# Performance work log

Hardware: AMD Instinct MI355X
Metric: run time of the kernel (lower is better)

The kernel has to match this reference:

```python
import jax, jax.numpy as jnp
import numpy as np

N_USER, N_TX, E = 50000, 50000, 600000
D_USER, D_TX, D_ALIGN, HID, OUT = 128, 64, 128, 256, 128


def setup_inputs() -> dict:
    key = jax.random.key(0)
    ks = jax.random.split(key, 16)
    s = 0.05
    return {
        "x_user": jax.random.normal(ks[0], (N_USER, D_USER), jnp.float32),
        "x_tx": jax.random.normal(ks[1], (N_TX, D_TX), jnp.float32),
        "edge_user_tx": jax.random.randint(ks[2], (2, E), 0, N_USER),
        "edge_tx_user": jax.random.randint(ks[3], (2, E), 0, N_TX),
        "W_align_user": jax.random.normal(ks[4], (D_USER, D_ALIGN), jnp.float32) * s,
        "b_align_user": jnp.zeros((D_ALIGN,), jnp.float32),
        "W_align_tx": jax.random.normal(ks[5], (D_TX, D_ALIGN), jnp.float32) * s,
        "b_align_tx": jnp.zeros((D_ALIGN,), jnp.float32),
        "eps_ut": jnp.zeros((), jnp.float32),
        "eps_tu": jnp.zeros((), jnp.float32),
        "W1_ut": jax.random.normal(ks[6], (D_TX + D_ALIGN, HID), jnp.float32) * s,
        "b1_ut": jnp.zeros((HID,), jnp.float32),
        "W2_ut": jax.random.normal(ks[7], (HID, OUT), jnp.float32) * s,
        "b2_ut": jnp.zeros((OUT,), jnp.float32),
        "W1_tu": jax.random.normal(ks[8], (D_USER + D_ALIGN, HID), jnp.float32) * s,
        "b1_tu": jnp.zeros((HID,), jnp.float32),
        "W2_tu": jax.random.normal(ks[9], (HID, OUT), jnp.float32) * s,
        "b2_tu": jnp.zeros((OUT,), jnp.float32),
    }


def _mlp(h, W1, b1, W2, b2):
    return jnp.maximum(h @ W1 + b1, 0.0) @ W2 + b2


def _hexgin_conv(x_src, x_dst, edge_index, W_a, b_a, eps, W1, b1, W2, b2):
    # align src features, gather along edges, scatter-sum into dst nodes
    a_src = x_src @ W_a + b_a                       # [N_src, D_ALIGN]
    msgs = a_src[edge_index[0]]                     # [E, D_ALIGN] gather
    agg = jax.ops.segment_sum(msgs, edge_index[1], num_segments=x_dst.shape[0])
    h = jnp.concatenate([(1.0 + eps) * x_dst, agg], axis=1)
    return _mlp(h, W1, b1, W2, b2)


def reference(x_user, x_tx, edge_user_tx, edge_tx_user,
              W_align_user, b_align_user, W_align_tx, b_align_tx,
              eps_ut, eps_tu,
              W1_ut, b1_ut, W2_ut, b2_ut,
              W1_tu, b1_tu, W2_tu, b2_tu):
    # relation (user, makes, tx): updates tx nodes
    out_tx = _hexgin_conv(x_user, x_tx, edge_user_tx,
                          W_align_user, b_align_user, eps_ut,
                          W1_ut, b1_ut, W2_ut, b2_ut)
    # relation (tx, to, user): updates user nodes
    out_user = _hexgin_conv(x_tx, x_user, edge_tx_user,
                            W_align_tx, b_align_tx, eps_tu,
                            W1_tu, b1_tu, W2_tu, b2_tu)
    # HeteroConv aggr='sum': single relation per target, so plain outputs
    return out_user, out_tx
```

## Files before the change

kernel.cpp:

```cpp
#include <hip/hip_runtime.h>
#include <hip/hip_bf16.h>


#define D_USER 128
#define D_TX 64
#define D_ALIGN 128
#define HID 256
#define OUT_D 128
#define NNODE 50000
#define BI 32
#define MAXSLOT 62
#define HPAD 264

typedef __attribute__((ext_vector_type(8))) short short8;
typedef __attribute__((ext_vector_type(4))) float f32x4;
typedef unsigned short ush;

__device__ __forceinline__ ush f2bf(float f) {
    union { float f; unsigned u; } v; v.f = f;
    unsigned u = v.u + 0x7fffu + ((v.u >> 16) & 1u);
    return (ush)(u >> 16);
}
__device__ __forceinline__ float2 bfu2f(unsigned u) {
    union { unsigned u; float f; } a, b;
    a.u = (u & 0xffffu) << 16;
    b.u = u & 0xffff0000u;
    return make_float2(a.f, b.f);
}
__device__ __forceinline__ unsigned f2bfu(float2 v) {
    return (unsigned)f2bf(v.x) | ((unsigned)f2bf(v.y) << 16);
}
__device__ __forceinline__ uint4 scale_bf8(uint4 v, float e) {
    unsigned* w = (unsigned*)&v;
    #pragma unroll
    for (int t = 0; t < 4; ++t) {
        float2 f = bfu2f(w[t]);
        w[t] = f2bfu(make_float2(f.x * e, f.y * e));
    }
    return v;
}


__device__ __forceinline__ void dev_fill(const int* __restrict__ e, int E, int i,
                                         int* __restrict__ pad, int dbase)
{
    int d = dbase + e[E + i];
    int s = e[i];
    int pos = atomicAdd(&pad[(size_t)d * BI], 1);
    if (pos < MAXSLOT)
        ((ush*)pad)[(size_t)d * (2 * BI) + 2 + pos] = (ush)s;
}

__device__ __forceinline__ void dev_prep(int b, int tid,
    const float* __restrict__ xu, ush* __restrict__ xbu,
    const float* __restrict__ xt, ush* __restrict__ xbt, int n8u, int n8t,
    const float* __restrict__ Wa_u, const float* __restrict__ ba_u,
    const float* __restrict__ W1_ut,
    const float* __restrict__ Wa_t, const float* __restrict__ ba_t,
    const float* __restrict__ W1_tu,
    const float* __restrict__ W2_ut, const float* __restrict__ W2_tu,
    ush* __restrict__ Bt1a, float* __restrict__ bfv1,
    ush* __restrict__ Bt1b, float* __restrict__ bfv2,
    ush* __restrict__ Bt2a, ush* __restrict__ Bt2b, int gb)
{
    if (b < gb) {
        int i = b * 256 + tid;
        const float* x; ush* xb; int j;
        if (i < n8u) { x = xu; xb = xbu; j = i; }
        else if (i < n8u + n8t) { x = xt; xb = xbt; j = i - n8u; }
        else return;
        const float4 a = *reinterpret_cast<const float4*>(&x[(size_t)j * 8]);
        const float4 c = *reinterpret_cast<const float4*>(&x[(size_t)j * 8 + 4]);
        ush o[8];
        o[0] = f2bf(a.x); o[1] = f2bf(a.y); o[2] = f2bf(a.z); o[3] = f2bf(a.w);
        o[4] = f2bf(c.x); o[5] = f2bf(c.y); o[6] = f2bf(c.z); o[7] = f2bf(c.w);
        *reinterpret_cast<uint4*>(&xb[(size_t)j * 8]) = *reinterpret_cast<uint4*>(o);
        return;
    }
    int idx = (b - gb) * 256 + tid;
    const int KT = 192;
    const int SEG1 = HID * (KT + 1);
    const int SEG2 = OUT_D * HID;
    if (idx < 2 * SEG1) {
        bool r2 = idx >= SEG1;
        int id = r2 ? idx - SEG1 : idx;
        const float* Wa = r2 ? Wa_t : Wa_u;
        const float* ba = r2 ? ba_t : ba_u;
        const float* W1 = r2 ? W1_tu : W1_ut;
        ush* Bt = r2 ? Bt1b : Bt1a;
        float* bfv = r2 ? bfv2 : bfv1;
        const int Dd = r2 ? 128 : 64;
        int c = id & (HID - 1);
        int k = id >> 8;
        const float* w1bot = W1 + (size_t)Dd * HID;
        if (k < Dd) {
            Bt[(size_t)c * KT + k] = f2bf(W1[(size_t)k * HID + c]);
        } else if (k < KT) {
            int ks = k - Dd;
            float acc = 0.f;
            for (int j = 0; j < D_ALIGN; ++j)
                acc += Wa[ks * D_ALIGN + j] * w1bot[(size_t)j * HID + c];
            Bt[(size_t)c * KT + k] = f2bf(acc);
        } else {
            float acc = 0.f;
            for (int j = 0; j < D_ALIGN; ++j)
                acc += ba[j] * w1bot[(size_t)j * HID + c];
            bfv[c] = acc;
        }
    } else if (idx < 2 * SEG1 + 2 * SEG2) {
        int id = idx - 2 * SEG1;
        bool r2 = id >= SEG2;
        if (r2) id -= SEG2;
        const float* W2 = r2 ? W2_tu : W2_ut;
        ush* Bt2 = r2 ? Bt2b : Bt2a;
        int c = id & (OUT_D - 1);
        int k = id >> 7;
        Bt2[(size_t)c * HID + k] = f2bf(W2[(size_t)k * OUT_D + c]);
    }
}

__device__ __forceinline__ int slot_word(const int* blk, int lane)
{
    return ((lane & 31) < 31) ? blk[1 + (lane & 31)] : 0;
}
__device__ __forceinline__ int slot_get(int word, int j)
{
    return (j & 1) ? ((word >> 16) & 0xffff) : (word & 0xffff);
}

__device__ __forceinline__ void dev_agg128(int w, int lane,
    const ush* __restrict__ xbu, const int* __restrict__ pad, ush* __restrict__ Sb1)
{
    const int* blk = pad + (size_t)w * BI;
    const int n = min(blk[0], MAXSLOT);
    const int word = slot_word(blk, lane);
    float2 acc = make_float2(0.f, 0.f);
    int i = 0;
    for (; i + 4 <= n; i += 4) {
        int wa = __shfl(word, i >> 1);
        int wb = __shfl(word, (i >> 1) + 1);
        int s0 = wa & 0xffff, s1 = (wa >> 16) & 0xffff;
        int s2 = wb & 0xffff, s3 = (wb >> 16) & 0xffff;
        unsigned v0 = *reinterpret_cast<const unsigned*>(&xbu[(size_t)s0 * 128 + 2 * lane]);
        unsigned v1 = *reinterpret_cast<const unsigned*>(&xbu[(size_t)s1 * 128 + 2 * lane]);
        unsigned v2 = *reinterpret_cast<const unsigned*>(&xbu[(size_t)s2 * 128 + 2 * lane]);
        unsigned v3 = *reinterpret_cast<const unsigned*>(&xbu[(size_t)s3 * 128 + 2 * lane]);
        float2 f0 = bfu2f(v0), f1 = bfu2f(v1), f2 = bfu2f(v2), f3 = bfu2f(v3);
        acc.x += (f0.x + f1.x) + (f2.x + f3.x);
        acc.y += (f0.y + f1.y) + (f2.y + f3.y);
    }
    for (; i < n; ++i) {
        int ww = __shfl(word, i >> 1);
        int s0 = slot_get(ww, i);
        unsigned v0 = *reinterpret_cast<const unsigned*>(&xbu[(size_t)s0 * 128 + 2 * lane]);
        float2 f0 = bfu2f(v0);
        acc.x += f0.x; acc.y += f0.y;
    }
    *reinterpret_cast<unsigned*>(&Sb1[(size_t)w * 128 + 2 * lane]) = f2bfu(acc);
}

__device__ __forceinline__ void dev_agg64(int w2, int lane,
    const ush* __restrict__ xbt, const int* __restrict__ pad, ush* __restrict__ Sb2)
{
    const int* blk = pad + (size_t)(NNODE + w2) * BI;
    const int n = min(blk[0], MAXSLOT);
    const int word = slot_word(blk, lane);
    const int half = lane >> 5, l2 = lane & 31;
    float2 acc = make_float2(0.f, 0.f);
    int i = 0;
    for (; i + 4 <= n; i += 4) {
        int ja = i + half, jb = i + 2 + half;
        int wa = __shfl(word, ja >> 1);
        int wb = __shfl(word, jb >> 1);
        int s0 = slot_get(wa, ja), s1 = slot_get(wb, jb);
        unsigned v0 = *reinterpret_cast<const unsigned*>(&xbt[(size_t)s0 * 64 + 2 * l2]);
        unsigned v1 = *reinterpret_cast<const unsigned*>(&xbt[(size_t)s1 * 64 + 2 * l2]);
        float2 f0 = bfu2f(v0), f1 = bfu2f(v1);
        acc.x += f0.x + f1.x;
        acc.y += f0.y + f1.y;
    }
    for (; i + 2 <= n; i += 2) {
        int j = i + half;
        int ww = __shfl(word, j >> 1);
        int s0 = slot_get(ww, j);
        unsigned v0 = *reinterpret_cast<const unsigned*>(&xbt[(size_t)s0 * 64 + 2 * l2]);
        float2 f0 = bfu2f(v0);
        acc.x += f0.x; acc.y += f0.y;
    }
    if (i < n && half == 0) {
        int ww = __shfl(word, i >> 1);
        int s0 = slot_get(ww, i);
        unsigned v0 = *reinterpret_cast<const unsigned*>(&xbt[(size_t)s0 * 64 + 2 * l2]);
        float2 f0 = bfu2f(v0);
        acc.x += f0.x; acc.y += f0.y;
    }
    acc.x += __shfl_xor(acc.x, 32);
    acc.y += __shfl_xor(acc.y, 32);
    if (half == 0)
        *reinterpret_cast<unsigned*>(&Sb2[(size_t)w2 * 64 + 2 * l2]) = f2bfu(acc);
}


__global__ __launch_bounds__(256) void kA(
    const int* __restrict__ e_ut, int E, int* __restrict__ pad,
    const float* __restrict__ xu, ush* __restrict__ xbu,
    const float* __restrict__ xt, ush* __restrict__ xbt, int n8u, int n8t,
    const float* __restrict__ Wa_u, const float* __restrict__ ba_u,
    const float* __restrict__ W1_ut,
    const float* __restrict__ Wa_t, const float* __restrict__ ba_t,
    const float* __restrict__ W1_tu,
    const float* __restrict__ W2_ut, const float* __restrict__ W2_tu,
    ush* __restrict__ Bt1a, float* __restrict__ bfv1,
    ush* __restrict__ Bt1b, float* __restrict__ bfv2,
    ush* __restrict__ Bt2a, ush* __restrict__ Bt2b, int gf, int gb)
{
    int b = blockIdx.x, tid = threadIdx.x;
    if (b < gf) {
        int i = b * 256 + tid;
        if (i < E) dev_fill(e_ut, E, i, pad, 0);
    } else {
        dev_prep(b - gf, tid, xu, xbu, xt, xbt, n8u, n8t,
                 Wa_u, ba_u, W1_ut, Wa_t, ba_t, W1_tu, W2_ut, W2_tu,
                 Bt1a, bfv1, Bt1b, bfv2, Bt2a, Bt2b, gb);
    }
}

__global__ __launch_bounds__(256) void kB(
    const int* __restrict__ e_tu, int E, int* __restrict__ pad,
    const ush* __restrict__ xbu, ush* __restrict__ Sb1, int gf)
{
    int b = blockIdx.x, tid = threadIdx.x;
    if (b < gf) {
        int i = b * 256 + tid;
        if (i < E) dev_fill(e_tu, E, i, pad, NNODE);
    } else {
        int w = (b - gf) * 4 + (tid >> 6);
        if (w < NNODE) dev_agg128(w, tid & 63, xbu, pad, Sb1);
    }
}

__global__ __launch_bounds__(256) void kC(
    const ush* __restrict__ xbt, const int* __restrict__ pad, ush* __restrict__ Sb2)
{
    int w2 = blockIdx.x * 4 + (threadIdx.x >> 6);
    if (w2 < NNODE) dev_agg64(w2, threadIdx.x & 63, xbt, pad, Sb2);
}

__global__ __launch_bounds__(256) void mlpF(
    const ush* __restrict__ xbt, const ush* __restrict__ xbu,
    const ush* __restrict__ Sb1, const ush* __restrict__ Sb2,
    const ush* __restrict__ Bt1a, const ush* __restrict__ Bt1b,
    const float* __restrict__ bfv1, const float* __restrict__ bfv2,
    const float* __restrict__ b1_ut, const float* __restrict__ b1_tu,
    const ush* __restrict__ Bt2a, const ush* __restrict__ Bt2b,
    const float* __restrict__ b2_ut, const float* __restrict__ b2_tu,
    const int* __restrict__ pad,
    const float* __restrict__ eps_ut, const float* __restrict__ eps_tu,
    float* __restrict__ out_tx, float* __restrict__ out_user, int M)
{
    __shared__ ush lds[27136];

    const int tid = threadIdx.x;
    const bool r2 = blockIdx.y != 0;
    const int bm = blockIdx.x * 64;
    const ush* xdst = r2 ? xbu : xbt;
    const int Dd = r2 ? 128 : 64;
    const ush* Sb = r2 ? Sb2 : Sb1;
    const int Dsrc = r2 ? 64 : 128;
    const ush* Bt1 = r2 ? Bt1b : Bt1a;
    const float* bfv = r2 ? bfv2 : bfv1;
    const float* b1 = r2 ? b1_tu : b1_ut;
    const ush* Bt2 = r2 ? Bt2b : Bt2a;
    const float* b2 = r2 ? b2_tu : b2_ut;
    const int* dgp = pad + (size_t)(r2 ? NNODE : 0) * BI;
    float* out = r2 ? out_user : out_tx;
    const float e = 1.f + (r2 ? eps_tu[0] : eps_ut[0]);

    const int lane = tid & 63, wn = tid >> 6;
    const int lo = lane & 15, hi = lane >> 4;
    const int KT1 = 192;

    const int sA_r = tid >> 2, sA_c8 = tid & 3;
    const int sB_c0 = tid >> 2, sB_ku = tid & 3;

    f32x4 acc[4][4];
    #pragma unroll
    for (int a = 0; a < 4; ++a)
        #pragma unroll
        for (int b = 0; b < 4; ++b)
            acc[a][b] = f32x4{0.f, 0.f, 0.f, 0.f};

    {
        const ush* src; int ld, kb;
        if (0 < Dd) { src = xdst; ld = Dd; kb = 0; }
        int gr = bm + sA_r;
        uint4 va = uint4{0u, 0u, 0u, 0u};
        if (gr < M)
            va = *reinterpret_cast<const uint4*>(&src[(size_t)gr * ld + kb + sA_c8 * 8]);
        va = scale_bf8(va, e);
        *reinterpret_cast<uint4*>(&lds[20480 + sA_r * 40 + sA_c8 * 8]) = va;
        #pragma unroll
        for (int q = 0; q < 4; ++q) {
            int c = sB_c0 + 64 * q;
            uint4 v = *reinterpret_cast<const uint4*>(&Bt1[(size_t)c * KT1 + sB_ku * 8]);
            *reinterpret_cast<uint4*>(&lds[c * 40 + sB_ku * 8]) = v;
        }
    }
    __syncthreads();

    #pragma unroll
    for (int k = 0; k < 6; ++k) {
        const int pOff  = (k & 1) ? 10240 : 0;
        const int pAOff = (k & 1) ? 23040 : 20480;
        const int nOff  = (k & 1) ? 0 : 10240;
        const int nAOff = (k & 1) ? 20480 : 23040;

        uint4 a_pf; uint4 b_pf[4];
        if (k < 5) {
            const int k0n = (k + 1) * 32;
            const ush* src; int ld, kb; bool sc;
            if (k0n < Dd) { src = xdst; ld = Dd; kb = k0n; sc = true; }
            else          { src = Sb;   ld = Dsrc; kb = k0n - Dd; sc = false; }
            int gr = bm + sA_r;
            a_pf = uint4{0u, 0u, 0u, 0u};
            if (gr < M)
                a_pf = *reinterpret_cast<const uint4*>(&src[(size_t)gr * ld + kb + sA_c8 * 8]);
            if (sc) a_pf = scale_bf8(a_pf, e);
            #pragma unroll
            for (int q = 0; q < 4; ++q) {
                int c = sB_c0 + 64 * q;
                b_pf[q] = *reinterpret_cast<const uint4*>(&Bt1[(size_t)c * KT1 + k0n + sB_ku * 8]);
            }
        }

        short8 av[4], bv[4];
        #pragma unroll
        for (int fi = 0; fi < 4; ++fi)
            av[fi] = *reinterpret_cast<const short8*>(&lds[pOff + (wn * 64 + fi * 16 + lo) * 40 + hi * 8]);
        #pragma unroll
        for (int fj = 0; fj < 4; ++fj)
            bv[fj] = *reinterpret_cast<const short8*>(&lds[pAOff + (fj * 16 + lo) * 40 + hi * 8]);
        #pragma unroll
        for (int fi = 0; fi < 4; ++fi)
            #pragma unroll
            for (int fj = 0; fj < 4; ++fj)
                acc[fi][fj] = __builtin_amdgcn_mfma_f32_16x16x32_bf16(av[fi], bv[fj], acc[fi][fj], 0, 0, 0);

        if (k < 5) {
            *reinterpret_cast<uint4*>(&lds[nAOff + sA_r * 40 + sA_c8 * 8]) = a_pf;
            #pragma unroll
            for (int q = 0; q < 4; ++q) {
                int c = sB_c0 + 64 * q;
                *reinterpret_cast<uint4*>(&lds[nOff + c * 40 + sB_ku * 8]) = b_pf[q];
            }
        }
        __syncthreads();
    }

    #pragma unroll
    for (int fi = 0; fi < 4; ++fi) {
        int colb = wn * 64 + fi * 16 + hi * 4;
        float4 b1v = *reinterpret_cast<const float4*>(&b1[colb]);
        float4 bfl = *reinterpret_cast<const float4*>(&bfv[colb]);
        #pragma unroll
        for (int fj = 0; fj < 4; ++fj) {
            int r = fj * 16 + lo;
            int gr = bm + r;
            float dgv = (gr < M) ? (float)dgp[(size_t)gr * BI] : 0.f;
            float v0 = fmaxf(acc[fi][fj][0] + b1v.x + dgv * bfl.x, 0.f);
            float v1 = fmaxf(acc[fi][fj][1] + b1v.y + dgv * bfl.y, 0.f);
            float v2 = fmaxf(acc[fi][fj][2] + b1v.z + dgv * bfl.z, 0.f);
            float v3 = fmaxf(acc[fi][fj][3] + b1v.w + dgv * bfl.w, 0.f);
            uint2 u;
            u.x = f2bfu(make_float2(v0, v1));
            u.y = f2bfu(make_float2(v2, v3));
            *reinterpret_cast<uint2*>(&lds[r * HPAD + colb]) = u;
        }
    }

    f32x4 acc2[2][4];
    #pragma unroll
    for (int a = 0; a < 2; ++a)
        #pragma unroll
        for (int b = 0; b < 4; ++b)
            acc2[a][b] = f32x4{0.f, 0.f, 0.f, 0.f};

    {
        #pragma unroll
        for (int q = 0; q < 2; ++q) {
            int c = sB_c0 + 64 * q;
            uint4 v = *reinterpret_cast<const uint4*>(&Bt2[(size_t)c * HID + sB_ku * 8]);
            *reinterpret_cast<uint4*>(&lds[16896 + c * 40 + sB_ku * 8]) = v;
        }
    }
    __syncthreads();

    #pragma unroll
    for (int k = 0; k < 8; ++k) {
        const int pOff = (k & 1) ? 22016 : 16896;
        const int nOff = (k & 1) ? 16896 : 22016;

        uint4 c_pf[2];
        if (k < 7) {
            const int k0n = (k + 1) * 32;
            #pragma unroll
            for (int q = 0; q < 2; ++q) {
                int c = sB_c0 + 64 * q;
                c_pf[q] = *reinterpret_cast<const uint4*>(&Bt2[(size_t)c * HID + k0n + sB_ku * 8]);
            }
        }

        short8 av2[2], bv2[4];
        #pragma unroll
        for (int fi = 0; fi < 2; ++fi)
            av2[fi] = *reinterpret_cast<const short8*>(&lds[pOff + (wn * 32 + fi * 16 + lo) * 40 + hi * 8]);
        #pragma unroll
        for (int fj = 0; fj < 4; ++fj)
            bv2[fj] = *reinterpret_cast<const short8*>(&lds[(fj * 16 + lo) * HPAD + k * 32 + hi * 8]);
        #pragma unroll
        for (int fi = 0; fi < 2; ++fi)
            #pragma unroll
            for (int fj = 0; fj < 4; ++fj)
                acc2[fi][fj] = __builtin_amdgcn_mfma_f32_16x16x32_bf16(av2[fi], bv2[fj], acc2[fi][fj], 0, 0, 0);

        if (k < 7) {
            #pragma unroll
            for (int q = 0; q < 2; ++q) {
                int c = sB_c0 + 64 * q;
                *reinterpret_cast<uint4*>(&lds[nOff + c * 40 + sB_ku * 8]) = c_pf[q];
            }
        }
        __syncthreads();
    }

    #pragma unroll
    for (int fi = 0; fi < 2; ++fi) {
        int colb = wn * 32 + fi * 16 + hi * 4;
        float4 b2v = *reinterpret_cast<const float4*>(&b2[colb]);
        #pragma unroll
        for (int fj = 0; fj < 4; ++fj) {
            int gr = bm + fj * 16 + lo;
            if (gr >= M) continue;
            float4 o;
            o.x = acc2[fi][fj][0] + b2v.x;
            o.y = acc2[fi][fj][1] + b2v.y;
            o.z = acc2[fi][fj][2] + b2v.z;
            o.w = acc2[fi][fj][3] + b2v.w;
            *reinterpret_cast<float4*>(&out[(size_t)gr * OUT_D + colb]) = o;
        }
    }
}

extern "C" void kernel_launch(void* const* d_in, const int* in_sizes, int n_in,
                              void* d_out, int out_size, void* d_ws, size_t ws_size,
                              hipStream_t stream)
{
    const float* x_user   = (const float*)d_in[0];
    const float* x_tx     = (const float*)d_in[1];
    const int*   e_ut     = (const int*)d_in[2];
    const int*   e_tu     = (const int*)d_in[3];
    const float* Wa_user  = (const float*)d_in[4];
    const float* ba_user  = (const float*)d_in[5];
    const float* Wa_tx    = (const float*)d_in[6];
    const float* ba_tx    = (const float*)d_in[7];
    const float* eps_ut   = (const float*)d_in[8];
    const float* eps_tu   = (const float*)d_in[9];
    const float* W1_ut    = (const float*)d_in[10];
    const float* b1_ut    = (const float*)d_in[11];
    const float* W2_ut    = (const float*)d_in[12];
    const float* b2_ut    = (const float*)d_in[13];
    const float* W1_tu    = (const float*)d_in[14];
    const float* b1_tu    = (const float*)d_in[15];
    const float* W2_tu    = (const float*)d_in[16];
    const float* b2_tu    = (const float*)d_in[17];

    const int N_user = in_sizes[0] / D_USER;
    const int N_tx   = in_sizes[1] / D_TX;
    const int E      = in_sizes[2] / 2;
    const int NT     = 2 * NNODE;

    float* out_user = (float*)d_out;
    float* out_tx   = (float*)d_out + (size_t)N_user * OUT_D;

    int*   pad   = (int*)d_ws;
    float* fws   = (float*)d_ws;
    ush*   Bt1a  = (ush*)(fws + 3300000);
    ush*   Bt1b  = (ush*)(fws + 3330000);
    ush*   Bt2a  = (ush*)(fws + 3360000);
    ush*   Bt2b  = (ush*)(fws + 3380000);
    float* bfv1  = fws + 3400000;
    float* bfv2  = fws + 3401000;
    ush*   xbu   = (ush*)(fws + 3410000);
    ush*   xbt   = (ush*)(fws + 6700000);
    ush*   Sb1   = (ush*)(fws + 8400000);
    ush*   Sb2   = (ush*)(fws + 11700000);

    const int threads = 256;
    const int n8u = N_user * D_USER / 8, n8t = N_tx * D_TX / 8;
    const int gf  = (E + 255) / 256;
    const int gb  = (n8u + n8t + 255) / 256;
    const int gw  = (2 * HID * 193 + 2 * OUT_D * HID + 255) / 256;
    const int ga  = (NNODE + 3) / 4;
    const int nbF = (NNODE + 63) / 64;

    hipMemsetAsync(pad, 0, (size_t)NT * BI * sizeof(int), stream);

    kA<<<gf + gb + gw, threads, 0, stream>>>(
        e_ut, E, pad, x_user, xbu, x_tx, xbt, n8u, n8t,
        Wa_user, ba_user, W1_ut, Wa_tx, ba_tx, W1_tu, W2_ut, W2_tu,
        Bt1a, bfv1, Bt1b, bfv2, Bt2a, Bt2b, gf, gb);

    kB<<<gf + ga, threads, 0, stream>>>(e_tu, E, pad, xbu, Sb1, gf);

    kC<<<ga, threads, 0, stream>>>(xbt, pad, Sb2);

    dim3 gF(nbF, 2);
    mlpF<<<gF, threads, 0, stream>>>(
        xbt, xbu, Sb1, Sb2, Bt1a, Bt1b, bfv1, bfv2, b1_ut, b1_tu,
        Bt2a, Bt2b, b2_ut, b2_tu, pad, eps_ut, eps_tu,
        out_tx, out_user, NNODE);
}
```

Measured before the change: 184.6 us.

## Enlarge fused MLP row tile to 128 rows with 512-thread blocks

The fused two-layer MLP kernel now processes 128 node rows per block with 8 waves arranged 2x4, instead of 64 rows with 4 waves. Each weight tile staged in shared memory is reused across twice as many rows, which halves weight traffic per output row and halves the block count. In exchange LDS use per block rises to about 88 KB, which may lower occupancy, and each block is bigger with fewer blocks per CU to hide latency.

```diff
diff --git a/kernel.cpp b/kernel.cpp
--- a/kernel.cpp
+++ b/kernel.cpp
@@ -10,7 +10,6 @@
 #define NNODE 50000
 #define BI 32
 #define MAXSLOT 62
-#define HPAD 264
 
 typedef __attribute__((ext_vector_type(8))) short short8;
 typedef __attribute__((ext_vector_type(4))) float f32x4;
@@ -246,7 +245,7 @@
     if (w2 < NNODE) dev_agg64(w2, threadIdx.x & 63, xbt, pad, Sb2);
 }
 
-__global__ __launch_bounds__(256) void mlpF(
+__global__ __launch_bounds__(512) void mlpF(
     const ush* __restrict__ xbt, const ush* __restrict__ xbu,
     const ush* __restrict__ Sb1, const ush* __restrict__ Sb2,
     const ush* __restrict__ Bt1a, const ush* __restrict__ Bt1b,
@@ -258,11 +257,11 @@
     const float* __restrict__ eps_ut, const float* __restrict__ eps_tu,
     float* __restrict__ out_tx, float* __restrict__ out_user, int M)
 {
-    __shared__ ush lds[27136];
+    __shared__ ush lds[44032];
 
     const int tid = threadIdx.x;
     const bool r2 = blockIdx.y != 0;
-    const int bm = blockIdx.x * 64;
+    const int bm = blockIdx.x * 128;
     const ush* xdst = r2 ? xbu : xbt;
     const int Dd = r2 ? 128 : 64;
     const ush* Sb = r2 ? Sb2 : Sb1;
@@ -276,8 +275,9 @@
     float* out = r2 ? out_user : out_tx;
     const float e = 1.f + (r2 ? eps_tu[0] : eps_ut[0]);
 
-    const int lane = tid & 63, wn = tid >> 6;
+    const int lane = tid & 63, wave = tid >> 6;
     const int lo = lane & 15, hi = lane >> 4;
+    const int wm = wave >> 2, wn = wave & 3;
     const int KT1 = 192;
 
     const int sA_r = tid >> 2, sA_c8 = tid & 3;
@@ -291,31 +291,29 @@
             acc[a][b] = f32x4{0.f, 0.f, 0.f, 0.f};
 
     {
-        const ush* src; int ld, kb;
-        if (0 < Dd) { src = xdst; ld = Dd; kb = 0; }
         int gr = bm + sA_r;
         uint4 va = uint4{0u, 0u, 0u, 0u};
         if (gr < M)
-            va = *reinterpret_cast<const uint4*>(&src[(size_t)gr * ld + kb + sA_c8 * 8]);
+            va = *reinterpret_cast<const uint4*>(&xdst[(size_t)gr * Dd + sA_c8 * 8]);
         va = scale_bf8(va, e);
-        *reinterpret_cast<uint4*>(&lds[20480 + sA_r * 40 + sA_c8 * 8]) = va;
-        #pragma unroll
-        for (int q = 0; q < 4; ++q) {
-            int c = sB_c0 + 64 * q;
+        *reinterpret_cast<uint4*>(&lds[sA_r * 40 + sA_c8 * 8]) = va;
+        #pragma unroll
+        for (int q = 0; q < 2; ++q) {
+            int c = sB_c0 + 128 * q;
             uint4 v = *reinterpret_cast<const uint4*>(&Bt1[(size_t)c * KT1 + sB_ku * 8]);
-            *reinterpret_cast<uint4*>(&lds[c * 40 + sB_ku * 8]) = v;
+            *reinterpret_cast<uint4*>(&lds[10240 + c * 40 + sB_ku * 8]) = v;
         }
     }
     __syncthreads();
 
     #pragma unroll
     for (int k = 0; k < 6; ++k) {
-        const int pOff  = (k & 1) ? 10240 : 0;
-        const int pAOff = (k & 1) ? 23040 : 20480;
-        const int nOff  = (k & 1) ? 0 : 10240;
-        const int nAOff = (k & 1) ? 20480 : 23040;
-
-        uint4 a_pf; uint4 b_pf[4];
+        const int pAOff = (k & 1) ? 5120 : 0;
+        const int nAOff = (k & 1) ? 0 : 5120;
+        const int pBOff = (k & 1) ? 20480 : 10240;
+        const int nBOff = (k & 1) ? 10240 : 20480;
+
+        uint4 a_pf; uint4 b_pf[2];
         if (k < 5) {
             const int k0n = (k + 1) * 32;
             const ush* src; int ld, kb; bool sc;
@@ -327,8 +325,8 @@
                 a_pf = *reinterpret_cast<const uint4*>(&src[(size_t)gr * ld + kb + sA_c8 * 8]);
             if (sc) a_pf = scale_bf8(a_pf, e);
             #pragma unroll
-            for (int q = 0; q < 4; ++q) {
-                int c = sB_c0 + 64 * q;
+            for (int q = 0; q < 2; ++q) {
+                int c = sB_c0 + 128 * q;
                 b_pf[q] = *reinterpret_cast<const uint4*>(&Bt1[(size_t)c * KT1 + k0n + sB_ku * 8]);
             }
         }
@@ -336,10 +334,12 @@
         short8 av[4], bv[4];
         #pragma unroll
         for (int fi = 0; fi < 4; ++fi)
-            av[fi] = *reinterpret_cast<const short8*>(&lds[pOff + (wn * 64 + fi * 16 + lo) * 40 + hi * 8]);
+            av[fi] = *reinterpret_cast<const short8*>(
+                &lds[pBOff + (wn * 64 + fi * 16 + lo) * 40 + hi * 8]);
         #pragma unroll
         for (int fj = 0; fj < 4; ++fj)
-            bv[fj] = *reinterpret_cast<const short8*>(&lds[pAOff + (fj * 16 + lo) * 40 + hi * 8]);
+            bv[fj] = *reinterpret_cast<const short8*>(
+                &lds[pAOff + (wm * 64 + fj * 16 + lo) * 40 + hi * 8]);
         #pragma unroll
         for (int fi = 0; fi < 4; ++fi)
             #pragma unroll
@@ -349,9 +349,9 @@
         if (k < 5) {
             *reinterpret_cast<uint4*>(&lds[nAOff + sA_r * 40 + sA_c8 * 8]) = a_pf;
             #pragma unroll
-            for (int q = 0; q < 4; ++q) {
-                int c = sB_c0 + 64 * q;
-                *reinterpret_cast<uint4*>(&lds[nOff + c * 40 + sB_ku * 8]) = b_pf[q];
+            for (int q = 0; q < 2; ++q) {
+                int c = sB_c0 + 128 * q;
+                *reinterpret_cast<uint4*>(&lds[nBOff + c * 40 + sB_ku * 8]) = b_pf[q];
             }
         }
         __syncthreads();
@@ -364,7 +364,7 @@
         float4 bfl = *reinterpret_cast<const float4*>(&bfv[colb]);
         #pragma unroll
         for (int fj = 0; fj < 4; ++fj) {
-            int r = fj * 16 + lo;
+            int r = wm * 64 + fj * 16 + lo;
             int gr = bm + r;
             float dgv = (gr < M) ? (float)dgp[(size_t)gr * BI] : 0.f;
             float v0 = fmaxf(acc[fi][fj][0] + b1v.x + dgv * bfl.x, 0.f);
@@ -374,7 +374,7 @@
             uint2 u;
             u.x = f2bfu(make_float2(v0, v1));
             u.y = f2bfu(make_float2(v2, v3));
-            *reinterpret_cast<uint2*>(&lds[r * HPAD + colb]) = u;
+            *reinterpret_cast<uint2*>(&lds[r * 264 + colb]) = u;
         }
     }
 
@@ -386,60 +386,51 @@
             acc2[a][b] = f32x4{0.f, 0.f, 0.f, 0.f};
 
     {
-        #pragma unroll
-        for (int q = 0; q < 2; ++q) {
-            int c = sB_c0 + 64 * q;
-            uint4 v = *reinterpret_cast<const uint4*>(&Bt2[(size_t)c * HID + sB_ku * 8]);
-            *reinterpret_cast<uint4*>(&lds[16896 + c * 40 + sB_ku * 8]) = v;
-        }
+        int c = sB_c0;
+        uint4 v = *reinterpret_cast<const uint4*>(&Bt2[(size_t)c * HID + sB_ku * 8]);
+        *reinterpret_cast<uint4*>(&lds[33792 + c * 40 + sB_ku * 8]) = v;
     }
     __syncthreads();
 
+    const int wn2 = wave & 3, wm2 = wave >> 2;
     #pragma unroll
     for (int k = 0; k < 8; ++k) {
-        const int pOff = (k & 1) ? 22016 : 16896;
-        const int nOff = (k & 1) ? 16896 : 22016;
-
-        uint4 c_pf[2];
+        const int pOff = (k & 1) ? 38912 : 33792;
+        const int nOff = (k & 1) ? 33792 : 38912;
+
+        uint4 c_pf;
         if (k < 7) {
             const int k0n = (k + 1) * 32;
-            #pragma unroll
-            for (int q = 0; q < 2; ++q) {
-                int c = sB_c0 + 64 * q;
-                c_pf[q] = *reinterpret_cast<const uint4*>(&Bt2[(size_t)c * HID + k0n + sB_ku * 8]);
-            }
+            c_pf = *reinterpret_cast<const uint4*>(&Bt2[(size_t)sB_c0 * HID + k0n + sB_ku * 8]);
         }
 
         short8 av2[2], bv2[4];
         #pragma unroll
         for (int fi = 0; fi < 2; ++fi)
-            av2[fi] = *reinterpret_cast<const short8*>(&lds[pOff + (wn * 32 + fi * 16 + lo) * 40 + hi * 8]);
+            av2[fi] = *reinterpret_cast<const short8*>(
+                &lds[pOff + (wn2 * 32 + fi * 16 + lo) * 40 + hi * 8]);
         #pragma unroll
         for (int fj = 0; fj < 4; ++fj)
-            bv2[fj] = *reinterpret_cast<const short8*>(&lds[(fj * 16 + lo) * HPAD + k * 32 + hi * 8]);
+            bv2[fj] = *reinterpret_cast<const short8*>(
+                &lds[(wm2 * 64 + fj * 16 + lo) * 264 + k * 32 + hi * 8]);
         #pragma unroll
         for (int fi = 0; fi < 2; ++fi)
             #pragma unroll
             for (int fj = 0; fj < 4; ++fj)
                 acc2[fi][fj] = __builtin_amdgcn_mfma_f32_16x16x32_bf16(av2[fi], bv2[fj], acc2[fi][fj], 0, 0, 0);
 
-        if (k < 7) {
-            #pragma unroll
-            for (int q = 0; q < 2; ++q) {
-                int c = sB_c0 + 64 * q;
-                *reinterpret_cast<uint4*>(&lds[nOff + c * 40 + sB_ku * 8]) = c_pf[q];
-            }
-        }
+        if (k < 7)
+            *reinterpret_cast<uint4*>(&lds[nOff + sB_c0 * 40 + sB_ku * 8]) = c_pf;
         __syncthreads();
     }
 
     #pragma unroll
     for (int fi = 0; fi < 2; ++fi) {
-        int colb = wn * 32 + fi * 16 + hi * 4;
+        int colb = wn2 * 32 + fi * 16 + hi * 4;
         float4 b2v = *reinterpret_cast<const float4*>(&b2[colb]);
         #pragma unroll
         for (int fj = 0; fj < 4; ++fj) {
-            int gr = bm + fj * 16 + lo;
+            int gr = bm + wm2 * 64 + fj * 16 + lo;
             if (gr >= M) continue;
             float4 o;
             o.x = acc2[fi][fj][0] + b2v.x;
@@ -501,7 +492,7 @@
     const int gb  = (n8u + n8t + 255) / 256;
     const int gw  = (2 * HID * 193 + 2 * OUT_D * HID + 255) / 256;
     const int ga  = (NNODE + 3) / 4;
-    const int nbF = (NNODE + 63) / 64;
+    const int nbF = (NNODE + 127) / 128;
 
     hipMemsetAsync(pad, 0, (size_t)NT * BI * sizeof(int), stream);
 
@@ -515,7 +506,7 @@
     kC<<<ga, threads, 0, stream>>>(xbt, pad, Sb2);
 
     dim3 gF(nbF, 2);
-    mlpF<<<gF, threads, 0, stream>>>(
+    mlpF<<<gF, 512, 0, stream>>>(
         xbt, xbu, Sb1, Sb2, Bt1a, Bt1b, bfv1, bfv2, b1_ut, b1_tu,
         Bt2a, Bt2b, b2_ut, b2_tu, pad, eps_ut, eps_tu,
         out_tx, out_user, NNODE);
```

New measurement: 189.0 us. +2.4%, slower.
